# Kernel tuning notes

Hardware: AMD Instinct MI355X
Metric: run time of the kernel (lower is better)

## Reference

```python
import jax, jax.numpy as jnp
import numpy as np

B, N, F_IN, T = 4, 512, 64, 16
K, F_CHEB, F_TIME, TS = 3, 64, 64, 1
E = 16384
LN_EPS = 1e-5


def setup_inputs() -> dict:
    key = jax.random.key(0)
    ks = jax.random.split(key, 18)
    s = 0.05
    X = jax.random.normal(ks[0], (B, N, F_IN, T), jnp.float32)
    # edges with guaranteed no self-loops (so remove_self_loops is a no-op)
    src = jax.random.randint(ks[1], (E,), 0, N, jnp.int32)
    off = jax.random.randint(ks[2], (E,), 1, N, jnp.int32)
    dst = (src + off) % N
    edge_index = jnp.stack([src, dst])
    return {
        'X': X,
        'edge_index': edge_index,
        'U1': jax.random.uniform(ks[3], (N,)) * s,
        'U2': jax.random.normal(ks[4], (F_IN, N)) * s,
        'U3': jax.random.uniform(ks[5], (F_IN,)) * s,
        'be': jax.random.normal(ks[6], (1, T, T)) * s,
        'Ve': jax.random.normal(ks[7], (T, T)) * s,
        'Ws1': jax.random.uniform(ks[8], (T,)) * s,
        'Ws2': jax.random.normal(ks[9], (F_IN, T)) * s,
        'Ws3': jax.random.uniform(ks[10], (F_IN,)) * s,
        'bs': jax.random.normal(ks[11], (1, N, N)) * s,
        'Vs': jax.random.normal(ks[12], (N, N)) * s,
        'W_cheb': jax.random.normal(ks[13], (K, F_IN, F_CHEB)) * s,
        'b_cheb': jax.random.uniform(ks[14], (F_CHEB,)) * s,
        'Wt': jax.random.normal(ks[15], (F_TIME, F_CHEB, 1, 3)) * s,
        'bt': jnp.zeros((F_TIME,), jnp.float32),
        'Wr': jax.random.normal(ks[16], (F_TIME, F_IN, 1, 1)) * s,
        'br': jnp.zeros((F_TIME,), jnp.float32),
        'gamma': jnp.ones((F_TIME,), jnp.float32),
        'beta': jnp.zeros((F_TIME,), jnp.float32),
    }


def _forward(edge_index, X, U1, U2, U3, be, Ve, Ws1, Ws2, Ws3, bs, Vs,
             W_cheb, b_cheb, Wt, bt, Wr, br, gamma, beta):
    Bn, Nn, Fn, Tn = X.shape
    # ---- temporal attention: (B,T,T)
    lhs_t = jnp.einsum('bnft,n->btf', X, U1) @ U2            # (B,T,N)
    rhs_t = jnp.einsum('f,bnft->bnt', U3, X)                 # (B,N,T)
    Et = jnp.matmul(Ve, jax.nn.sigmoid(jnp.matmul(lhs_t, rhs_t) + be))
    Et = jax.nn.softmax(Et, axis=1)
    # temporally re-weighted signal
    Xt = jnp.matmul(X.reshape(Bn, Nn * Fn, Tn), Et).reshape(Bn, Nn, Fn, Tn)
    # ---- spatial attention: (B,N,N)
    lhs_s = jnp.einsum('bnft,t->bnf', Xt, Ws1) @ Ws2         # (B,N,T)
    rhs_s = jnp.einsum('f,bnft->btn', Ws3, Xt)               # (B,T,N)
    S = jnp.matmul(Vs, jax.nn.sigmoid(jnp.matmul(lhs_s, rhs_s) + bs))
    S = jax.nn.softmax(S, axis=1)                            # (B,N,N)
    # ---- scaled sym-normalized Laplacian; lambda_max=2 so 2/lambda_max = 1.
    # edges: -D^-1/2 A D^-1/2 (E), +I self loops (N), then add_self_loops(-1) (N)
    row, col = edge_index[0], edge_index[1]
    ew = jnp.ones(row.shape, X.dtype)
    deg = jnp.zeros((Nn,), X.dtype).at[row].add(ew)
    dis = jnp.where(deg > 0, 1.0 / jnp.sqrt(jnp.maximum(deg, 1.0)), 0.0)  # deg is integral so max() only guards deg==0
    wn = -dis[row] * dis[col]
    loops = jnp.arange(Nn)
    rows = jnp.concatenate([row, loops, loops])
    cols = jnp.concatenate([col, loops, loops])
    norm = jnp.concatenate([wn, jnp.ones((Nn,), X.dtype), -jnp.ones((Nn,), X.dtype)])
    att_norm = norm[None, :] * S[:, rows, cols]              # (B,Etot)

    def prop(h, w):
        # propagate over transposed edges: gather at col, scatter-add at row
        # h: (B,T,N,F); w broadcastable to (B,1,Etot)
        msg = w[..., None] * h[:, :, cols, :]
        return jnp.zeros_like(h).at[:, :, rows, :].add(msg)

    xt = X.transpose(0, 3, 1, 2)                             # (B,T,N,F): ChebConv applied per timestep
    Tx0 = jnp.diagonal(S, axis1=1, axis2=2)[:, None, :, None] * xt  # diag(S) @ x
    out = jnp.einsum('btnf,fg->btng', Tx0, W_cheb[0])
    if W_cheb.shape[0] > 1:
        Tx1 = prop(Tx0, att_norm[:, None, :])
        out = out + jnp.einsum('btnf,fg->btng', Tx1, W_cheb[1])
    for k in range(2, W_cheb.shape[0]):
        Tx2 = 2.0 * prop(Tx1, norm[None, None, :]) - Tx0
        out = out + jnp.einsum('btnf,fg->btng', Tx2, W_cheb[k])
        Tx0, Tx1 = Tx1, Tx2
    X_hat = jax.nn.relu(out + b_cheb)                        # (B,T,N,Fc)
    # ---- time conv (1x3, stride (1,TS)) on (B,Fc,N,T) + residual 1x1 conv
    conv_t = jax.lax.conv_general_dilated(
        X_hat.transpose(0, 3, 2, 1), Wt, (1, TS), ((0, 0), (1, 1)),
        dimension_numbers=('NCHW', 'OIHW', 'NCHW')) + bt[None, :, None, None]
    conv_r = jax.lax.conv_general_dilated(
        X.transpose(0, 2, 1, 3), Wr, (1, TS), ((0, 0), (0, 0)),
        dimension_numbers=('NCHW', 'OIHW', 'NCHW')) + br[None, :, None, None]
    Z = jax.nn.relu(conv_r + conv_t).transpose(0, 3, 2, 1)   # (B,T,N,Ft)
    mu = jnp.mean(Z, -1, keepdims=True)
    var = jnp.var(Z, -1, keepdims=True)
    Z = (Z - mu) / jnp.sqrt(var + LN_EPS) * gamma + beta     # LayerNorm over Ft
    return Z.transpose(0, 2, 3, 1)                           # (B,N,Ft,T)


def reference(X, edge_index, U1, U2, U3, be, Ve, Ws1, Ws2, Ws3, bs, Vs,
              W_cheb, b_cheb, Wt, bt, Wr, br, gamma, beta):
    return _forward(edge_index, X, U1, U2, U3, be, Ve, Ws1, Ws2, Ws3, bs, Vs,
                    W_cheb, b_cheb, Wt, bt, Wr, br, gamma, beta)
```

## Files before the change

### kernel.cpp

```cpp
#include <hip/hip_runtime.h>
#include <math.h>

#define NB 4
#define NV 512
#define NF 64
#define NT 16
#define NE 16384

#define TX1_OFF    2097152u
#define TX2_OFF    4194304u
#define XHAT_OFF   6291456u
#define ST_OFF     TX1_OFF
#define SIGT_OFF   TX2_OFF
#define BST_OFF    8388608u
#define ET_OFF     8650752u
#define PART_OFF   8651776u
#define RHST_OFF   8684544u
#define LHSS_OFF   8717312u
#define RHSSN_OFF  8750080u
#define DIAGS_OFF  8782848u
#define WSATT_OFF  8784896u
#define CSRW_OFF   8850432u
#define WTT_OFF    8866816u
#define WRT_OFF    8879104u
#define DIS_OFF    8883200u
#define RHS3_OFF   8883712u
#define EW1_OFF    8916480u
#define FEND       8916544u

__global__ void k_hist(const int* __restrict__ row, int* __restrict__ counts) {
    __shared__ int h[512];
    int c = blockIdx.x, i = threadIdx.x;
    h[i] = 0; h[i + 256] = 0;
    __syncthreads();
    atomicAdd(&h[row[c * 256 + i]], 1);
    __syncthreads();
    counts[c * 512 + i] = h[i];
    counts[c * 512 + i + 256] = h[i + 256];
}

__global__ void k_scan2(int* __restrict__ counts, float* __restrict__ dis,
                        int* __restrict__ row_start) {
    __shared__ int sc[512];
    int r = threadIdx.x;
    int sum = 0;
    for (int c = 0; c < 64; ++c) {
        int v = counts[c * 512 + r];
        counts[c * 512 + r] = sum;
        sum += v;
    }
    dis[r] = sum > 0 ? 1.0f / sqrtf((float)sum) : 0.0f;
    sc[r] = sum;
    __syncthreads();
    for (int off = 1; off < 512; off <<= 1) {
        int v = sc[r];
        int add = (r >= off) ? sc[r - off] : 0;
        __syncthreads();
        sc[r] = v + add;
        __syncthreads();
    }
    int incl = sc[r];
    row_start[r] = incl - sum;
    if (r == 511) row_start[512] = incl;
}

__global__ void k_fill2(const int* __restrict__ ei, const int* __restrict__ counts,
                        const int* __restrict__ row_start, const float* __restrict__ dis,
                        int* __restrict__ csr_col, int* __restrict__ csr_row,
                        float* __restrict__ csr_w) {
    __shared__ int rowL[256];
    int c = blockIdx.x, i = threadIdx.x;
    int e = c * 256 + i;
    int r = ei[e];
    int col = ei[NE + e];
    rowL[i] = r;
    __syncthreads();
    int rank = 0;
    for (int j = 0; j < 256; ++j)
        if (j < i && rowL[j] == r) rank++;
    int pos = row_start[r] + counts[c * 512 + r] + rank;
    csr_col[pos] = col;
    csr_row[pos] = r;
    csr_w[pos] = -dis[r] * dis[col];
}

__global__ void k_wtrans(const float* __restrict__ Wt, const float* __restrict__ Wr,
                         const float* __restrict__ bs,
                         float* __restrict__ WtT, float* __restrict__ WrT,
                         float* __restrict__ bsT) {
    __shared__ float tile[64][65];
    int bid = blockIdx.x;
    if (bid < 64) {
        int r0 = (bid >> 3) * 64, c0 = (bid & 7) * 64;
        int c = threadIdx.x & 63, rq = threadIdx.x >> 6;
        for (int k = 0; k < 16; ++k) {
            int r = rq * 16 + k;
            tile[r][c] = bs[(r0 + r) * 512 + c0 + c];
        }
        __syncthreads();
        int r2 = threadIdx.x & 63;
        for (int k = 0; k < 16; ++k) {
            int c2 = rq * 16 + k;
            bsT[(size_t)(c0 + c2) * 512 + r0 + r2] = tile[r2][c2];
        }
    } else {
        int idx = (bid - 64) * 256 + threadIdx.x;
        if (idx < 12288) {
            int o = idx & 63, gd = idx >> 6;
            int g = gd / 3, dt = gd - g * 3;
            WtT[idx] = Wt[(o * 64 + g) * 3 + dt];
        } else if (idx < 16384) {
            int i2 = idx - 12288;
            int o = i2 & 63, f = i2 >> 6;
            WrT[i2] = Wr[o * 64 + f];
        }
    }
}

__global__ void k_xin(const float* __restrict__ X, const float* __restrict__ U1,
                      const float* __restrict__ U3, const float* __restrict__ Ws3,
                      float* __restrict__ part, float* __restrict__ rhs,
                      float* __restrict__ rhs3) {
    int bid = blockIdx.x;
    int tid = threadIdx.x;
    if (bid < 32) {
        int b = bid >> 3, g = bid & 7;
        float acc[4] = {0.f, 0.f, 0.f, 0.f};
        const float* Xb = X + (size_t)b * NV * 1024;
        int n0 = g * 64;
        for (int nn = 0; nn < 64; ++nn) {
            int n = n0 + nn;
            float u = U1[n];
            const float* xp = Xb + (size_t)n * 1024;
#pragma unroll
            for (int k = 0; k < 4; ++k) acc[k] += xp[tid + 256 * k] * u;
        }
#pragma unroll
        for (int k = 0; k < 4; ++k) part[(size_t)(b * 8 + g) * 1024 + tid + 256 * k] = acc[k];
    } else {
        int gid = (bid - 32) * 256 + tid;
        int t = gid & 15;
        const float* xp = X + ((size_t)(gid >> 4)) * 1024 + t;
        float a = 0.f, a3 = 0.f;
#pragma unroll
        for (int f = 0; f < 64; ++f) {
            float v = xp[f * 16];
            a += U3[f] * v;
            a3 += Ws3[f] * v;
        }
        rhs[gid] = a;
        rhs3[gid] = a3;
    }
}

__global__ void k_temporal(const float* __restrict__ part, const float* __restrict__ rhs_g,
                           const float* __restrict__ U2, const float* __restrict__ be,
                           const float* __restrict__ Ve, const float* __restrict__ Ws1,
                           float* __restrict__ Et, float* __restrict__ ew1) {
    __shared__ float lhs1[1024];
    __shared__ float rhsL[8192];
    __shared__ float M[1024];
    __shared__ float Esig[256];
    __shared__ float Et0[256];
    __shared__ float red[32];
    __shared__ float EtL[256];
    int b = blockIdx.x, tid = threadIdx.x;
#pragma unroll
    for (int k = 0; k < 4; ++k) {
        int idx = tid + 256 * k;
        float s = 0.f;
        for (int g = 0; g < 8; ++g) s += part[(size_t)(b * 8 + g) * 1024 + idx];
        lhs1[idx] = s;
    }
    for (int k = 0; k < 32; ++k) rhsL[tid + 256 * k] = rhs_g[(size_t)b * 8192 + tid + 256 * k];
    __syncthreads();
    {
        float acc[4] = {0.f, 0.f, 0.f, 0.f};
        int fA[4], tA[4];
#pragma unroll
        for (int k = 0; k < 4; ++k) { int idx = tid + 256 * k; fA[k] = idx >> 4; tA[k] = idx & 15; }
        for (int n = 0; n < 512; ++n) {
#pragma unroll
            for (int k = 0; k < 4; ++k) acc[k] += U2[fA[k] * 512 + n] * rhsL[n * 16 + tA[k]];
        }
#pragma unroll
        for (int k = 0; k < 4; ++k) M[tid + 256 * k] = acc[k];
    }
    __syncthreads();
    {
        int t1 = tid >> 4, t2 = tid & 15;
        float s = 0.f;
        for (int f = 0; f < 64; ++f) s += lhs1[f * 16 + t1] * M[f * 16 + t2];
        s += be[t1 * 16 + t2];
        Esig[tid] = 1.f / (1.f + expf(-s));
    }
    __syncthreads();
    {
        int t1 = tid >> 4, t2 = tid & 15;
        float s = 0.f;
        for (int k = 0; k < 16; ++k) s += Ve[t1 * 16 + k] * Esig[k * 16 + t2];
        Et0[tid] = s;
    }
    __syncthreads();
    if (tid < 16) {
        float m = -1e30f;
        for (int k = 0; k < 16; ++k) m = fmaxf(m, Et0[k * 16 + tid]);
        float s = 0.f;
        for (int k = 0; k < 16; ++k) s += expf(Et0[k * 16 + tid] - m);
        red[tid] = m; red[16 + tid] = 1.f / s;
    }
    __syncthreads();
    {
        int t2 = tid & 15;
        float etv = expf(Et0[tid] - red[t2]) * red[16 + t2];
        Et[b * 256 + tid] = etv;
        EtL[tid] = etv;
    }
    __syncthreads();
    if (tid < 16) {
        float s = 0.f;
        for (int t = 0; t < 16; ++t) s += EtL[tid * 16 + t] * Ws1[t];
        ew1[b * 16 + tid] = s;
    }
}

__global__ __launch_bounds__(256) void k_spat2(const float* __restrict__ X,
                                               const float* __restrict__ ew1,
                                               const float* __restrict__ rhs3,
                                               const float* __restrict__ Et,
                                               const float* __restrict__ Ws2,
                                               float* __restrict__ lhs_s,
                                               float* __restrict__ rhs_sn) {
    int wv = threadIdx.x >> 6, lane = threadIdx.x & 63;
    int bn = blockIdx.x * 4 + wv;
    int b = bn >> 9;
    const float4* xp = (const float4*)(X + (size_t)bn * 1024 + lane * 16);
    float4 x0 = xp[0], x1 = xp[1], x2 = xp[2], x3 = xp[3];
    const float* e1 = ew1 + b * 16;
    float l1 = x0.x * e1[0] + x0.y * e1[1] + x0.z * e1[2] + x0.w * e1[3]
             + x1.x * e1[4] + x1.y * e1[5] + x1.z * e1[6] + x1.w * e1[7]
             + x2.x * e1[8] + x2.y * e1[9] + x2.z * e1[10] + x2.w * e1[11]
             + x3.x * e1[12] + x3.y * e1[13] + x3.z * e1[14] + x3.w * e1[15];
    const float4* wp = (const float4*)(Ws2 + lane * 16);
    float4 w0 = wp[0], w1 = wp[1], w2 = wp[2], w3 = wp[3];
    float p[16] = {l1 * w0.x, l1 * w0.y, l1 * w0.z, l1 * w0.w,
                   l1 * w1.x, l1 * w1.y, l1 * w1.z, l1 * w1.w,
                   l1 * w2.x, l1 * w2.y, l1 * w2.z, l1 * w2.w,
                   l1 * w3.x, l1 * w3.y, l1 * w3.z, l1 * w3.w};
#pragma unroll
    for (int off = 32; off; off >>= 1) {
#pragma unroll
        for (int k = 0; k < 16; ++k) p[k] += __shfl_xor(p[k], off);
    }
    if (lane == 0) {
        float4* lp = (float4*)(lhs_s + (size_t)bn * 16);
        lp[0] = make_float4(p[0], p[1], p[2], p[3]);
        lp[1] = make_float4(p[4], p[5], p[6], p[7]);
        lp[2] = make_float4(p[8], p[9], p[10], p[11]);
        lp[3] = make_float4(p[12], p[13], p[14], p[15]);
    }
    if (lane < 16) {
        const float* r3 = rhs3 + (size_t)bn * 16;
        const float* Eb = Et + b * 256;
        float s = 0.f;
#pragma unroll
        for (int tp = 0; tp < 16; ++tp) s += r3[tp] * Eb[tp * 16 + lane];
        rhs_sn[(size_t)bn * 16 + lane] = s;
    }
}

__global__ void k_sigT(const float* __restrict__ lhs_s, const float* __restrict__ rhs_sn,
                       const float* __restrict__ bsT, float* __restrict__ sigT) {
    int gid = blockIdx.x * 256 + threadIdx.x;
    int k = gid & 511, j = (gid >> 9) & 511, b = gid >> 18;
    const float4* lp = (const float4*)(lhs_s + (size_t)(b * 512 + k) * 16);
    const float4* rp = (const float4*)(rhs_sn + (size_t)(b * 512 + j) * 16);
    float s = 0.f;
#pragma unroll
    for (int q = 0; q < 4; ++q) {
        float4 a = lp[q], c = rp[q];
        s += a.x * c.x + a.y * c.y + a.z * c.z + a.w * c.w;
    }
    s += bsT[(size_t)j * 512 + k];
    sigT[gid] = 1.f / (1.f + expf(-s));
}

__global__ __launch_bounds__(256) void k_gemm_s(const float* __restrict__ sigT,
                                                const float* __restrict__ Vs,
                                                float* __restrict__ S0T) {
    __shared__ float As[32 * 68];
    __shared__ float Bs[32 * 68];
    int bI = blockIdx.x, bJ = blockIdx.y, b = blockIdx.z;
    int tid = threadIdx.x, tx = tid & 15, ty = tid >> 4;
    float acc[4][4] = {};
    const float* Ab = sigT + ((size_t)b * 512 + bJ * 64) * 512;
    const float* Bb = Vs + (size_t)bI * 64 * 512;
    for (int k0 = 0; k0 < 512; k0 += 32) {
#pragma unroll
        for (int p = 0; p < 2; ++p) {
            int idx = tid + 256 * p;
            int row = idx >> 3, kk = (idx & 7) * 4;
            float4 a = *(const float4*)(Ab + (size_t)row * 512 + k0 + kk);
            As[(kk + 0) * 68 + row] = a.x; As[(kk + 1) * 68 + row] = a.y;
            As[(kk + 2) * 68 + row] = a.z; As[(kk + 3) * 68 + row] = a.w;
            float4 v = *(const float4*)(Bb + (size_t)row * 512 + k0 + kk);
            Bs[(kk + 0) * 68 + row] = v.x; Bs[(kk + 1) * 68 + row] = v.y;
            Bs[(kk + 2) * 68 + row] = v.z; Bs[(kk + 3) * 68 + row] = v.w;
        }
        __syncthreads();
#pragma unroll
        for (int kk = 0; kk < 32; ++kk) {
            float4 a = *(const float4*)(As + kk * 68 + ty * 4);
            float4 bv = *(const float4*)(Bs + kk * 68 + tx * 4);
            acc[0][0] += a.x * bv.x; acc[0][1] += a.x * bv.y; acc[0][2] += a.x * bv.z; acc[0][3] += a.x * bv.w;
            acc[1][0] += a.y * bv.x; acc[1][1] += a.y * bv.y; acc[1][2] += a.y * bv.z; acc[1][3] += a.y * bv.w;
            acc[2][0] += a.z * bv.x; acc[2][1] += a.z * bv.y; acc[2][2] += a.z * bv.z; acc[2][3] += a.z * bv.w;
            acc[3][0] += a.w * bv.x; acc[3][1] += a.w * bv.y; acc[3][2] += a.w * bv.z; acc[3][3] += a.w * bv.w;
        }
        __syncthreads();
    }
    float* Cb = S0T + ((size_t)b * 512 + bJ * 64) * 512 + bI * 64;
#pragma unroll
    for (int y = 0; y < 4; ++y) {
        int j = ty * 4 + y;
        *(float4*)(Cb + (size_t)j * 512 + tx * 4) =
            make_float4(acc[y][0], acc[y][1], acc[y][2], acc[y][3]);
    }
}

__global__ void k_softmax_s(float* __restrict__ ST, float* __restrict__ diagS) {
    __shared__ float red[4];
    int bj = blockIdx.x;
    int b = bj >> 9, j = bj & 511;
    float* row = ST + (size_t)bj * 512;
    int tid = threadIdx.x;
    float v0 = row[tid], v1 = row[tid + 256];
    float m = fmaxf(v0, v1);
    for (int off = 32; off; off >>= 1) m = fmaxf(m, __shfl_xor(m, off));
    if ((tid & 63) == 0) red[tid >> 6] = m;
    __syncthreads();
    m = fmaxf(fmaxf(red[0], red[1]), fmaxf(red[2], red[3]));
    __syncthreads();
    float e0 = expf(v0 - m), e1 = expf(v1 - m);
    float s = e0 + e1;
    for (int off = 32; off; off >>= 1) s += __shfl_xor(s, off);
    if ((tid & 63) == 0) red[tid >> 6] = s;
    __syncthreads();
    s = red[0] + red[1] + red[2] + red[3];
    float inv = 1.f / s;
    float r0 = e0 * inv, r1 = e1 * inv;
    row[tid] = r0;
    row[tid + 256] = r1;
    if (j < 256) { if (tid == j) diagS[b * 512 + j] = r0; }
    else { if (tid == j - 256) diagS[b * 512 + j] = r1; }
}

__global__ void k_wS(const int* __restrict__ csr_col, const int* __restrict__ csr_row,
                     const float* __restrict__ csr_w, const float* __restrict__ ST,
                     const float* __restrict__ diagS, float* __restrict__ wS) {
    int gid = blockIdx.x * 256 + threadIdx.x;
    int pos = gid & (NE - 1), b = gid >> 14;
    int c = csr_col[pos], r = csr_row[pos];
    wS[gid] = csr_w[pos] * ST[((size_t)(b * 512 + c)) * 512 + r] * diagS[b * 512 + c];
}

__global__ __launch_bounds__(256) void k_prop1(const float* __restrict__ X,
                                               const float* __restrict__ wS,
                                               const int* __restrict__ csr_col,
                                               const int* __restrict__ row_start,
                                               float* __restrict__ Tx1) {
    int logical = ((blockIdx.x & 7) << 8) + (blockIdx.x >> 3);
    int b = logical >> 9, tile = (logical >> 7) & 3, rq = logical & 127;
    int w = threadIdx.x >> 6, lane = threadIdx.x & 63;
    int i = rq * 4 + w;
    int s = row_start[i], e2 = row_start[i + 1];
    const float* Xb = X + (size_t)b * 512 * 1024 + tile * 256 + lane * 4;
    const float* wb = wS + (size_t)b * NE;
    float4 acc = make_float4(0.f, 0.f, 0.f, 0.f);
    for (int p = s; p < e2; ++p) {
        int col = csr_col[p];
        float wv = wb[p];
        float4 v = *(const float4*)(Xb + (size_t)col * 1024);
        acc.x += wv * v.x; acc.y += wv * v.y; acc.z += wv * v.z; acc.w += wv * v.w;
    }
    *(float4*)(Tx1 + ((size_t)(b * 512 + i)) * 1024 + tile * 256 + lane * 4) = acc;
}

__global__ __launch_bounds__(256) void k_prop2(const float* __restrict__ Tx1,
                                               const float* __restrict__ X,
                                               const float* __restrict__ diagS,
                                               const float* __restrict__ csr_w,
                                               const int* __restrict__ csr_col,
                                               const int* __restrict__ row_start,
                                               float* __restrict__ Tx2) {
    int logical = ((blockIdx.x & 7) << 8) + (blockIdx.x >> 3);
    int b = logical >> 9, tile = (logical >> 7) & 3, rq = logical & 127;
    int w = threadIdx.x >> 6, lane = threadIdx.x & 63;
    int i = rq * 4 + w;
    int s = row_start[i], e2 = row_start[i + 1];
    const float* T1b = Tx1 + (size_t)b * 512 * 1024 + tile * 256 + lane * 4;
    float4 acc = make_float4(0.f, 0.f, 0.f, 0.f);
    for (int p = s; p < e2; ++p) {
        int col = csr_col[p];
        float wv = csr_w[p];
        float4 v = *(const float4*)(T1b + (size_t)col * 1024);
        acc.x += wv * v.x; acc.y += wv * v.y; acc.z += wv * v.z; acc.w += wv * v.w;
    }
    float ds = diagS[b * 512 + i];
    size_t off = ((size_t)(b * 512 + i)) * 1024 + tile * 256 + lane * 4;
    float4 x0 = *(const float4*)(X + off);
    float4 o;
    o.x = 2.f * acc.x - ds * x0.x;
    o.y = 2.f * acc.y - ds * x0.y;
    o.z = 2.f * acc.z - ds * x0.z;
    o.w = 2.f * acc.w - ds * x0.w;
    *(float4*)(Tx2 + off) = o;
}

__global__ __launch_bounds__(256) void k_cheb(const float* __restrict__ X,
                                              const float* __restrict__ Tx1,
                                              const float* __restrict__ Tx2,
                                              const float* __restrict__ diagS,
                                              const float* __restrict__ Wc,
                                              const float* __restrict__ bc,
                                              float* __restrict__ Xh) {
    __shared__ float t0s[4][1024], t1s[4][1024], t2s[4][1024];
    int bn0 = blockIdx.x * 4;
    int tid = threadIdx.x;
    int r = tid >> 6, l = tid & 63;
    int bn = bn0 + r;
    float ds = diagS[bn];
    const float4* xp = (const float4*)(X + (size_t)bn * 1024);
    const float4* p1 = (const float4*)(Tx1 + (size_t)bn * 1024);
    const float4* p2 = (const float4*)(Tx2 + (size_t)bn * 1024);
#pragma unroll
    for (int k = 0; k < 4; ++k) {
        float4 v = xp[k * 64 + l];
        v.x *= ds; v.y *= ds; v.z *= ds; v.w *= ds;
        ((float4*)t0s[r])[k * 64 + l] = v;
        ((float4*)t1s[r])[k * 64 + l] = p1[k * 64 + l];
        ((float4*)t2s[r])[k * 64 + l] = p2[k * 64 + l];
    }
    __syncthreads();
    int g4 = (l & 15) * 4, t4 = (l >> 4) * 4;
    float4 bv = *(const float4*)(bc + g4);
    float4 acc0 = make_float4(bv.x, bv.x, bv.x, bv.x);
    float4 acc1 = make_float4(bv.y, bv.y, bv.y, bv.y);
    float4 acc2 = make_float4(bv.z, bv.z, bv.z, bv.z);
    float4 acc3 = make_float4(bv.w, bv.w, bv.w, bv.w);
    const float* t0r = t0s[r];
    const float* t1r = t1s[r];
    const float* t2r = t2s[r];
    for (int f = 0; f < 64; ++f) {
        float4 a0 = *(const float4*)(t0r + f * 16 + t4);
        float4 a1 = *(const float4*)(t1r + f * 16 + t4);
        float4 a2 = *(const float4*)(t2r + f * 16 + t4);
        float4 w0 = *(const float4*)(Wc + f * 64 + g4);
        float4 w1 = *(const float4*)(Wc + 4096 + f * 64 + g4);
        float4 w2 = *(const float4*)(Wc + 8192 + f * 64 + g4);
        acc0.x += w0.x * a0.x + w1.x * a1.x + w2.x * a2.x;
        acc0.y += w0.x * a0.y + w1.x * a1.y + w2.x * a2.y;
        acc0.z += w0.x * a0.z + w1.x * a1.z + w2.x * a2.z;
        acc0.w += w0.x * a0.w + w1.x * a1.w + w2.x * a2.w;
        acc1.x += w0.y * a0.x + w1.y * a1.x + w2.y * a2.x;
        acc1.y += w0.y * a0.y + w1.y * a1.y + w2.y * a2.y;
        acc1.z += w0.y * a0.z + w1.y * a1.z + w2.y * a2.z;
        acc1.w += w0.y * a0.w + w1.y * a1.w + w2.y * a2.w;
        acc2.x += w0.z * a0.x + w1.z * a1.x + w2.z * a2.x;
        acc2.y += w0.z * a0.y + w1.z * a1.y + w2.z * a2.y;
        acc2.z += w0.z * a0.z + w1.z * a1.z + w2.z * a2.z;
        acc2.w += w0.z * a0.w + w1.z * a1.w + w2.z * a2.w;
        acc3.x += w0.w * a0.x + w1.w * a1.x + w2.w * a2.x;
        acc3.y += w0.w * a0.y + w1.w * a1.y + w2.w * a2.y;
        acc3.z += w0.w * a0.z + w1.w * a1.z + w2.w * a2.z;
        acc3.w += w0.w * a0.w + w1.w * a1.w + w2.w * a2.w;
    }
    float* op = Xh + (size_t)bn * 1024;
    float4 o0, o1, o2, o3;
    o0.x = fmaxf(acc0.x, 0.f); o0.y = fmaxf(acc0.y, 0.f); o0.z = fmaxf(acc0.z, 0.f); o0.w = fmaxf(acc0.w, 0.f);
    o1.x = fmaxf(acc1.x, 0.f); o1.y = fmaxf(acc1.y, 0.f); o1.z = fmaxf(acc1.z, 0.f); o1.w = fmaxf(acc1.w, 0.f);
    o2.x = fmaxf(acc2.x, 0.f); o2.y = fmaxf(acc2.y, 0.f); o2.z = fmaxf(acc2.z, 0.f); o2.w = fmaxf(acc2.w, 0.f);
    o3.x = fmaxf(acc3.x, 0.f); o3.y = fmaxf(acc3.y, 0.f); o3.z = fmaxf(acc3.z, 0.f); o3.w = fmaxf(acc3.w, 0.f);
    *(float4*)(op + (g4 + 0) * 16 + t4) = o0;
    *(float4*)(op + (g4 + 1) * 16 + t4) = o1;
    *(float4*)(op + (g4 + 2) * 16 + t4) = o2;
    *(float4*)(op + (g4 + 3) * 16 + t4) = o3;
}

__global__ __launch_bounds__(256) void k_out(const float* __restrict__ X,
                                             const float* __restrict__ Xh,
                                             const float* __restrict__ WtT,
                                             const float* __restrict__ WrT,
                                             const float* __restrict__ bt,
                                             const float* __restrict__ br,
                                             const float* __restrict__ gamma,
                                             const float* __restrict__ beta,
                                             float* __restrict__ out) {
    __shared__ float xh[64 * 20];
    __shared__ float xl[64 * 16];
    __shared__ float red[4160];
    int bn = blockIdx.x;
    int tid = threadIdx.x;
    int o = tid & 63, q = tid >> 6;
    {
        int g = tid & 63, s4 = tid >> 6;
        int slot = (s4 == 0) ? 0 : 16 + s4;
        xh[g * 20 + slot] = 0.f;
    }
    {
        float4 v = ((const float4*)(Xh + (size_t)bn * 1024))[tid];
        int g = tid >> 2, t0 = (tid & 3) * 4;
        xh[g * 20 + t0 + 1] = v.x;
        xh[g * 20 + t0 + 2] = v.y;
        xh[g * 20 + t0 + 3] = v.z;
        xh[g * 20 + t0 + 4] = v.w;
        float4 u = ((const float4*)(X + (size_t)bn * 1024))[tid];
        *(float4*)(xl + tid * 4) = u;
    }
    __syncthreads();
    float acc[16];
#pragma unroll
    for (int k = 0; k < 16; ++k) acc[k] = 0.f;
    for (int gi = 0; gi < 16; ++gi) {
        int g = q * 16 + gi;
        const float4* xp = (const float4*)(xh + g * 20);
        float4 xa = xp[0], xb = xp[1], xc = xp[2], xd = xp[3], xe = xp[4];
        float xs[20] = {xa.x, xa.y, xa.z, xa.w, xb.x, xb.y, xb.z, xb.w,
                        xc.x, xc.y, xc.z, xc.w, xd.x, xd.y, xd.z, xd.w,
                        xe.x, xe.y, xe.z, xe.w};
        float w0 = WtT[(g * 3 + 0) * 64 + o];
        float w1 = WtT[(g * 3 + 1) * 64 + o];
        float w2 = WtT[(g * 3 + 2) * 64 + o];
#pragma unroll
        for (int tt = 0; tt < 16; ++tt)
            acc[tt] += xs[tt] * w0 + xs[tt + 1] * w1 + xs[tt + 2] * w2;
    }
    for (int fi = 0; fi < 16; ++fi) {
        int f = q * 16 + fi;
        const float4* xp = (const float4*)(xl + f * 16);
        float4 xa = xp[0], xb = xp[1], xc = xp[2], xd = xp[3];
        float xs[16] = {xa.x, xa.y, xa.z, xa.w, xb.x, xb.y, xb.z, xb.w,
                        xc.x, xc.y, xc.z, xc.w, xd.x, xd.y, xd.z, xd.w};
        float w = WrT[f * 64 + o];
#pragma unroll
        for (int tt = 0; tt < 16; ++tt) acc[tt] += xs[tt] * w;
    }
#pragma unroll
    for (int tt = 0; tt < 16; ++tt) red[q * 1024 + tt * 64 + o] = acc[tt];
    __syncthreads();
    float bsum = bt[o] + br[o];
    float go = gamma[o], bo = beta[o];
    float zv4[4];
#pragma unroll
    for (int tt = 0; tt < 4; ++tt) {
        int t = q * 4 + tt;
        float s = bsum;
#pragma unroll
        for (int qq = 0; qq < 4; ++qq) s += red[qq * 1024 + t * 64 + o];
        zv4[tt] = fmaxf(s, 0.f);
    }
    __syncthreads();
#pragma unroll
    for (int tt = 0; tt < 4; ++tt) {
        int t = q * 4 + tt;
        float zv = zv4[tt];
        float s = zv, sq = zv * zv;
        for (int off = 32; off; off >>= 1) {
            s += __shfl_xor(s, off);
            sq += __shfl_xor(sq, off);
        }
        float mu = s * (1.f / 64.f);
        float var = sq * (1.f / 64.f) - mu * mu;
        red[t * 65 + o] = (zv - mu) * rsqrtf(var + 1e-5f) * go + bo;
    }
    __syncthreads();
#pragma unroll
    for (int k = 0; k < 4; ++k) {
        int i = tid + 256 * k;
        out[(size_t)bn * 1024 + i] = red[(i & 15) * 65 + (i >> 4)];
    }
}

extern "C" void kernel_launch(void* const* d_in, const int* in_sizes, int n_in,
                              void* d_out, int out_size, void* d_ws, size_t ws_size,
                              hipStream_t stream) {
    const float* X     = (const float*)d_in[0];
    const int*   ei    = (const int*)d_in[1];
    const float* U1    = (const float*)d_in[2];
    const float* U2    = (const float*)d_in[3];
    const float* U3    = (const float*)d_in[4];
    const float* be    = (const float*)d_in[5];
    const float* Ve    = (const float*)d_in[6];
    const float* Ws1   = (const float*)d_in[7];
    const float* Ws2   = (const float*)d_in[8];
    const float* Ws3   = (const float*)d_in[9];
    const float* bs    = (const float*)d_in[10];
    const float* Vs    = (const float*)d_in[11];
    const float* Wc    = (const float*)d_in[12];
    const float* bc    = (const float*)d_in[13];
    const float* Wt    = (const float*)d_in[14];
    const float* bt    = (const float*)d_in[15];
    const float* Wr    = (const float*)d_in[16];
    const float* br    = (const float*)d_in[17];
    const float* gamma = (const float*)d_in[18];
    const float* beta  = (const float*)d_in[19];

    float* ws = (float*)d_ws;
    float* Tx1    = ws + TX1_OFF;
    float* Tx2    = ws + TX2_OFF;
    float* Xh     = ws + XHAT_OFF;
    float* ST     = ws + ST_OFF;
    float* sigT   = ws + SIGT_OFF;
    float* bsT    = ws + BST_OFF;
    float* Et     = ws + ET_OFF;
    float* part   = ws + PART_OFF;
    float* rhs_t  = ws + RHST_OFF;
    float* lhs_s  = ws + LHSS_OFF;
    float* rhs_sn = ws + RHSSN_OFF;
    float* diagS  = ws + DIAGS_OFF;
    float* wS     = ws + WSATT_OFF;
    float* csr_w  = ws + CSRW_OFF;
    float* WtT    = ws + WTT_OFF;
    float* WrT    = ws + WRT_OFF;
    float* dis    = ws + DIS_OFF;
    float* rhs3   = ws + RHS3_OFF;
    float* ew1    = ws + EW1_OFF;

    int* ib        = (int*)(ws + FEND);
    int* row_start = ib;
    int* csr_col   = ib + 516;
    int* csr_row   = csr_col + NE;
    int* counts    = csr_row + NE;

    k_hist<<<64, 256, 0, stream>>>(ei, counts);
    k_scan2<<<1, 512, 0, stream>>>(counts, dis, row_start);
    k_fill2<<<64, 256, 0, stream>>>(ei, counts, row_start, dis, csr_col, csr_row, csr_w);

    k_wtrans<<<128, 256, 0, stream>>>(Wt, Wr, bs, WtT, WrT, bsT);

    k_xin<<<160, 256, 0, stream>>>(X, U1, U3, Ws3, part, rhs_t, rhs3);
    k_temporal<<<4, 256, 0, stream>>>(part, rhs_t, U2, be, Ve, Ws1, Et, ew1);

    k_spat2<<<512, 256, 0, stream>>>(X, ew1, rhs3, Et, Ws2, lhs_s, rhs_sn);
    k_sigT<<<4096, 256, 0, stream>>>(lhs_s, rhs_sn, bsT, sigT);
    k_gemm_s<<<dim3(8, 8, 4), 256, 0, stream>>>(sigT, Vs, ST);
    k_softmax_s<<<2048, 256, 0, stream>>>(ST, diagS);
    k_wS<<<256, 256, 0, stream>>>(csr_col, csr_row, csr_w, ST, diagS, wS);

    k_prop1<<<2048, 256, 0, stream>>>(X, wS, csr_col, row_start, Tx1);
    k_prop2<<<2048, 256, 0, stream>>>(Tx1, X, diagS, csr_w, csr_col, row_start, Tx2);
    k_cheb<<<512, 256, 0, stream>>>(X, Tx1, Tx2, diagS, Wc, bc, Xh);

    k_out<<<2048, 256, 0, stream>>>(X, Xh, WtT, WrT, bt, br, gamma, beta, (float*)d_out);
}
```

Baseline: 181.2 us.

## Fuse prop2, Chebyshev combine and output conv into one tail kernel; merge prep kernels

```diff
diff --git a/kernel.cpp b/kernel.cpp
--- a/kernel.cpp
+++ b/kernel.cpp
@@ -9,7 +9,6 @@
 
 #define TX1_OFF    2097152u
 #define TX2_OFF    4194304u
-#define XHAT_OFF   6291456u
 #define ST_OFF     TX1_OFF
 #define SIGT_OFF   TX2_OFF
 #define BST_OFF    8388608u
@@ -28,15 +27,82 @@
 #define EW1_OFF    8916480u
 #define FEND       8916544u
 
-__global__ void k_hist(const int* __restrict__ row, int* __restrict__ counts) {
+__global__ void k_prep(const int* __restrict__ ei, int* __restrict__ counts,
+                       const float* __restrict__ Wt, const float* __restrict__ Wr,
+                       const float* __restrict__ bs,
+                       float* __restrict__ WtT, float* __restrict__ WrT,
+                       float* __restrict__ bsT,
+                       const float* __restrict__ X, const float* __restrict__ U1,
+                       const float* __restrict__ U3, const float* __restrict__ Ws3,
+                       float* __restrict__ part, float* __restrict__ rhs,
+                       float* __restrict__ rhs3) {
     __shared__ int h[512];
-    int c = blockIdx.x, i = threadIdx.x;
-    h[i] = 0; h[i + 256] = 0;
-    __syncthreads();
-    atomicAdd(&h[row[c * 256 + i]], 1);
-    __syncthreads();
-    counts[c * 512 + i] = h[i];
-    counts[c * 512 + i + 256] = h[i + 256];
+    __shared__ float tile[64][65];
+    int bid = blockIdx.x, tid = threadIdx.x;
+    if (bid < 64) {
+        int c = bid;
+        h[tid] = 0; h[tid + 256] = 0;
+        __syncthreads();
+        atomicAdd(&h[ei[c * 256 + tid]], 1);
+        __syncthreads();
+        counts[c * 512 + tid] = h[tid];
+        counts[c * 512 + tid + 256] = h[tid + 256];
+    } else if (bid < 128) {
+        int tb = bid - 64;
+        int r0 = (tb >> 3) * 64, c0 = (tb & 7) * 64;
+        int c = tid & 63, rq = tid >> 6;
+        for (int k = 0; k < 16; ++k) {
+            int r = rq * 16 + k;
+            tile[r][c] = bs[(r0 + r) * 512 + c0 + c];
+        }
+        __syncthreads();
+        int r2 = tid & 63;
+        for (int k = 0; k < 16; ++k) {
+            int c2 = rq * 16 + k;
+            bsT[(size_t)(c0 + c2) * 512 + r0 + r2] = tile[r2][c2];
+        }
+    } else if (bid < 192) {
+        int idx = (bid - 128) * 256 + tid;
+        if (idx < 12288) {
+            int o = idx & 63, gd = idx >> 6;
+            int g = gd / 3, dt = gd - g * 3;
+            WtT[idx] = Wt[(o * 64 + g) * 3 + dt];
+        } else {
+            int i2 = idx - 12288;
+            int o = i2 & 63, f = i2 >> 6;
+            WrT[i2] = Wr[o * 64 + f];
+        }
+    } else {
+        int sub = bid - 192;
+        if (sub < 32) {
+            int b = sub >> 3, g = sub & 7;
+            float acc[4] = {0.f, 0.f, 0.f, 0.f};
+            const float* Xb = X + (size_t)b * NV * 1024;
+            int n0 = g * 64;
+            for (int nn = 0; nn < 64; ++nn) {
+                int n = n0 + nn;
+                float u = U1[n];
+                const float* xp = Xb + (size_t)n * 1024;
+#pragma unroll
+                for (int k = 0; k < 4; ++k) acc[k] += xp[tid + 256 * k] * u;
+            }
+#pragma unroll
+            for (int k = 0; k < 4; ++k) part[(size_t)(b * 8 + g) * 1024 + tid + 256 * k] = acc[k];
+        } else {
+            int gid = (sub - 32) * 256 + tid;
+            int t = gid & 15;
+            const float* xp = X + ((size_t)(gid >> 4)) * 1024 + t;
+            float a = 0.f, a3 = 0.f;
+#pragma unroll
+            for (int f = 0; f < 64; ++f) {
+                float v = xp[f * 16];
+                a += U3[f] * v;
+                a3 += Ws3[f] * v;
+            }
+            rhs[gid] = a;
+            rhs3[gid] = a3;
+        }
+    }
 }
 
 __global__ void k_scan2(int* __restrict__ counts, float* __restrict__ dis,
@@ -82,75 +148,6 @@
     csr_col[pos] = col;
     csr_row[pos] = r;
     csr_w[pos] = -dis[r] * dis[col];
-}
-
-__global__ void k_wtrans(const float* __restrict__ Wt, const float* __restrict__ Wr,
-                         const float* __restrict__ bs,
-                         float* __restrict__ WtT, float* __restrict__ WrT,
-                         float* __restrict__ bsT) {
-    __shared__ float tile[64][65];
-    int bid = blockIdx.x;
-    if (bid < 64) {
-        int r0 = (bid >> 3) * 64, c0 = (bid & 7) * 64;
-        int c = threadIdx.x & 63, rq = threadIdx.x >> 6;
-        for (int k = 0; k < 16; ++k) {
-            int r = rq * 16 + k;
-            tile[r][c] = bs[(r0 + r) * 512 + c0 + c];
-        }
-        __syncthreads();
-        int r2 = threadIdx.x & 63;
-        for (int k = 0; k < 16; ++k) {
-            int c2 = rq * 16 + k;
-            bsT[(size_t)(c0 + c2) * 512 + r0 + r2] = tile[r2][c2];
-        }
-    } else {
-        int idx = (bid - 64) * 256 + threadIdx.x;
-        if (idx < 12288) {
-            int o = idx & 63, gd = idx >> 6;
-            int g = gd / 3, dt = gd - g * 3;
-            WtT[idx] = Wt[(o * 64 + g) * 3 + dt];
-        } else if (idx < 16384) {
-            int i2 = idx - 12288;
-            int o = i2 & 63, f = i2 >> 6;
-            WrT[i2] = Wr[o * 64 + f];
-        }
-    }
-}
-
-__global__ void k_xin(const float* __restrict__ X, const float* __restrict__ U1,
-                      const float* __restrict__ U3, const float* __restrict__ Ws3,
-                      float* __restrict__ part, float* __restrict__ rhs,
-                      float* __restrict__ rhs3) {
-    int bid = blockIdx.x;
-    int tid = threadIdx.x;
-    if (bid < 32) {
-        int b = bid >> 3, g = bid & 7;
-        float acc[4] = {0.f, 0.f, 0.f, 0.f};
-        const float* Xb = X + (size_t)b * NV * 1024;
-        int n0 = g * 64;
-        for (int nn = 0; nn < 64; ++nn) {
-            int n = n0 + nn;
-            float u = U1[n];
-            const float* xp = Xb + (size_t)n * 1024;
-#pragma unroll
-            for (int k = 0; k < 4; ++k) acc[k] += xp[tid + 256 * k] * u;
-        }
-#pragma unroll
-        for (int k = 0; k < 4; ++k) part[(size_t)(b * 8 + g) * 1024 + tid + 256 * k] = acc[k];
-    } else {
-        int gid = (bid - 32) * 256 + tid;
-        int t = gid & 15;
-        const float* xp = X + ((size_t)(gid >> 4)) * 1024 + t;
-        float a = 0.f, a3 = 0.f;
-#pragma unroll
-        for (int f = 0; f < 64; ++f) {
-            float v = xp[f * 16];
-            a += U3[f] * v;
-            a3 += Ws3[f] * v;
-        }
-        rhs[gid] = a;
-        rhs3[gid] = a3;
-    }
 }
 
 __global__ void k_temporal(const float* __restrict__ part, const float* __restrict__ rhs_g,
@@ -386,19 +383,31 @@
     *(float4*)(Tx1 + ((size_t)(b * 512 + i)) * 1024 + tile * 256 + lane * 4) = acc;
 }
 
-__global__ __launch_bounds__(256) void k_prop2(const float* __restrict__ Tx1,
-                                               const float* __restrict__ X,
-                                               const float* __restrict__ diagS,
-                                               const float* __restrict__ csr_w,
-                                               const int* __restrict__ csr_col,
-                                               const int* __restrict__ row_start,
-                                               float* __restrict__ Tx2) {
-    int logical = ((blockIdx.x & 7) << 8) + (blockIdx.x >> 3);
-    int b = logical >> 9, tile = (logical >> 7) & 3, rq = logical & 127;
-    int w = threadIdx.x >> 6, lane = threadIdx.x & 63;
-    int i = rq * 4 + w;
+__global__ __launch_bounds__(256) void k_tail(const float* __restrict__ X,
+                                              const float* __restrict__ Tx1,
+                                              const float* __restrict__ diagS,
+                                              const float* __restrict__ csr_w,
+                                              const int* __restrict__ csr_col,
+                                              const int* __restrict__ row_start,
+                                              const float* __restrict__ Wc,
+                                              const float* __restrict__ bc,
+                                              const float* __restrict__ WtT,
+                                              const float* __restrict__ WrT,
+                                              const float* __restrict__ bt,
+                                              const float* __restrict__ br,
+                                              const float* __restrict__ gamma,
+                                              const float* __restrict__ beta,
+                                              float* __restrict__ out) {
+    __shared__ float t0s[1024], t1s[1024], t2s[1024], xl[1024];
+    __shared__ float xh[1280];
+    __shared__ float red[4160];
+    int blk = ((blockIdx.x & 7) << 8) + (blockIdx.x >> 3);
+    int b = blk >> 9, i = blk & 511;
+    int tid = threadIdx.x;
+#pragma unroll
+    for (int k = 0; k < 5; ++k) xh[tid + 256 * k] = 0.f;
     int s = row_start[i], e2 = row_start[i + 1];
-    const float* T1b = Tx1 + (size_t)b * 512 * 1024 + tile * 256 + lane * 4;
+    const float* T1b = Tx1 + (size_t)b * 512 * 1024 + tid * 4;
     float4 acc = make_float4(0.f, 0.f, 0.f, 0.f);
     for (int p = s; p < e2; ++p) {
         int col = csr_col[p];
@@ -406,121 +415,47 @@
         float4 v = *(const float4*)(T1b + (size_t)col * 1024);
         acc.x += wv * v.x; acc.y += wv * v.y; acc.z += wv * v.z; acc.w += wv * v.w;
     }
-    float ds = diagS[b * 512 + i];
-    size_t off = ((size_t)(b * 512 + i)) * 1024 + tile * 256 + lane * 4;
-    float4 x0 = *(const float4*)(X + off);
-    float4 o;
-    o.x = 2.f * acc.x - ds * x0.x;
-    o.y = 2.f * acc.y - ds * x0.y;
-    o.z = 2.f * acc.z - ds * x0.z;
-    o.w = 2.f * acc.w - ds * x0.w;
-    *(float4*)(Tx2 + off) = o;
-}
-
-__global__ __launch_bounds__(256) void k_cheb(const float* __restrict__ X,
-                                              const float* __restrict__ Tx1,
-                                              const float* __restrict__ Tx2,
-                                              const float* __restrict__ diagS,
-                                              const float* __restrict__ Wc,
-                                              const float* __restrict__ bc,
-                                              float* __restrict__ Xh) {
-    __shared__ float t0s[4][1024], t1s[4][1024], t2s[4][1024];
-    int bn0 = blockIdx.x * 4;
-    int tid = threadIdx.x;
-    int r = tid >> 6, l = tid & 63;
-    int bn = bn0 + r;
-    float ds = diagS[bn];
-    const float4* xp = (const float4*)(X + (size_t)bn * 1024);
-    const float4* p1 = (const float4*)(Tx1 + (size_t)bn * 1024);
-    const float4* p2 = (const float4*)(Tx2 + (size_t)bn * 1024);
-#pragma unroll
-    for (int k = 0; k < 4; ++k) {
-        float4 v = xp[k * 64 + l];
-        v.x *= ds; v.y *= ds; v.z *= ds; v.w *= ds;
-        ((float4*)t0s[r])[k * 64 + l] = v;
-        ((float4*)t1s[r])[k * 64 + l] = p1[k * 64 + l];
-        ((float4*)t2s[r])[k * 64 + l] = p2[k * 64 + l];
-    }
-    __syncthreads();
-    int g4 = (l & 15) * 4, t4 = (l >> 4) * 4;
-    float4 bv = *(const float4*)(bc + g4);
-    float4 acc0 = make_float4(bv.x, bv.x, bv.x, bv.x);
-    float4 acc1 = make_float4(bv.y, bv.y, bv.y, bv.y);
-    float4 acc2 = make_float4(bv.z, bv.z, bv.z, bv.z);
-    float4 acc3 = make_float4(bv.w, bv.w, bv.w, bv.w);
-    const float* t0r = t0s[r];
-    const float* t1r = t1s[r];
-    const float* t2r = t2s[r];
-    for (int f = 0; f < 64; ++f) {
-        float4 a0 = *(const float4*)(t0r + f * 16 + t4);
-        float4 a1 = *(const float4*)(t1r + f * 16 + t4);
-        float4 a2 = *(const float4*)(t2r + f * 16 + t4);
-        float4 w0 = *(const float4*)(Wc + f * 64 + g4);
-        float4 w1 = *(const float4*)(Wc + 4096 + f * 64 + g4);
-        float4 w2 = *(const float4*)(Wc + 8192 + f * 64 + g4);
-        acc0.x += w0.x * a0.x + w1.x * a1.x + w2.x * a2.x;
-        acc0.y += w0.x * a0.y + w1.x * a1.y + w2.x * a2.y;
-        acc0.z += w0.x * a0.z + w1.x * a1.z + w2.x * a2.z;
-        acc0.w += w0.x * a0.w + w1.x * a1.w + w2.x * a2.w;
-        acc1.x += w0.y * a0.x + w1.y * a1.x + w2.y * a2.x;
-        acc1.y += w0.y * a0.y + w1.y * a1.y + w2.y * a2.y;
-        acc1.z += w0.y * a0.z + w1.y * a1.z + w2.y * a2.z;
-        acc1.w += w0.y * a0.w + w1.y * a1.w + w2.y * a2.w;
-        acc2.x += w0.z * a0.x + w1.z * a1.x + w2.z * a2.x;
-        acc2.y += w0.z * a0.y + w1.z * a1.y + w2.z * a2.y;
-        acc2.z += w0.z * a0.z + w1.z * a1.z + w2.z * a2.z;
-        acc2.w += w0.z * a0.w + w1.z * a1.w + w2.z * a2.w;
-        acc3.x += w0.w * a0.x + w1.w * a1.x + w2.w * a2.x;
-        acc3.y += w0.w * a0.y + w1.w * a1.y + w2.w * a2.y;
-        acc3.z += w0.w * a0.z + w1.w * a1.z + w2.w * a2.z;
-        acc3.w += w0.w * a0.w + w1.w * a1.w + w2.w * a2.w;
-    }
-    float* op = Xh + (size_t)bn * 1024;
-    float4 o0, o1, o2, o3;
-    o0.x = fmaxf(acc0.x, 0.f); o0.y = fmaxf(acc0.y, 0.f); o0.z = fmaxf(acc0.z, 0.f); o0.w = fmaxf(acc0.w, 0.f);
-    o1.x = fmaxf(acc1.x, 0.f); o1.y = fmaxf(acc1.y, 0.f); o1.z = fmaxf(acc1.z, 0.f); o1.w = fmaxf(acc1.w, 0.f);
-    o2.x = fmaxf(acc2.x, 0.f); o2.y = fmaxf(acc2.y, 0.f); o2.z = fmaxf(acc2.z, 0.f); o2.w = fmaxf(acc2.w, 0.f);
-    o3.x = fmaxf(acc3.x, 0.f); o3.y = fmaxf(acc3.y, 0.f); o3.z = fmaxf(acc3.z, 0.f); o3.w = fmaxf(acc3.w, 0.f);
-    *(float4*)(op + (g4 + 0) * 16 + t4) = o0;
-    *(float4*)(op + (g4 + 1) * 16 + t4) = o1;
-    *(float4*)(op + (g4 + 2) * 16 + t4) = o2;
-    *(float4*)(op + (g4 + 3) * 16 + t4) = o3;
-}
-
-__global__ __launch_bounds__(256) void k_out(const float* __restrict__ X,
-                                             const float* __restrict__ Xh,
-                                             const float* __restrict__ WtT,
-                                             const float* __restrict__ WrT,
-                                             const float* __restrict__ bt,
-                                             const float* __restrict__ br,
-                                             const float* __restrict__ gamma,
-                                             const float* __restrict__ beta,
-                                             float* __restrict__ out) {
-    __shared__ float xh[64 * 20];
-    __shared__ float xl[64 * 16];
-    __shared__ float red[4160];
-    int bn = blockIdx.x;
-    int tid = threadIdx.x;
+    float ds = diagS[blk];
+    size_t roff = (size_t)blk * 1024 + tid * 4;
+    float4 x0 = *(const float4*)(X + roff);
+    float4 t1v = *(const float4*)(Tx1 + roff);
+    float4 t2v, t0v;
+    t2v.x = 2.f * acc.x - ds * x0.x;
+    t2v.y = 2.f * acc.y - ds * x0.y;
+    t2v.z = 2.f * acc.z - ds * x0.z;
+    t2v.w = 2.f * acc.w - ds * x0.w;
+    t0v.x = ds * x0.x; t0v.y = ds * x0.y; t0v.z = ds * x0.z; t0v.w = ds * x0.w;
+    *(float4*)(xl  + tid * 4) = x0;
+    *(float4*)(t0s + tid * 4) = t0v;
+    *(float4*)(t1s + tid * 4) = t1v;
+    *(float4*)(t2s + tid * 4) = t2v;
+    __syncthreads();
+    {
+        int g4 = (tid & 15) * 4, t = tid >> 4;
+        float4 bv = *(const float4*)(bc + g4);
+        float4 accg = bv;
+        for (int f = 0; f < 64; ++f) {
+            float a0 = t0s[f * 16 + t];
+            float a1 = t1s[f * 16 + t];
+            float a2 = t2s[f * 16 + t];
+            float4 w0 = *(const float4*)(Wc + f * 64 + g4);
+            float4 w1 = *(const float4*)(Wc + 4096 + f * 64 + g4);
+            float4 w2 = *(const float4*)(Wc + 8192 + f * 64 + g4);
+            accg.x += w0.x * a0 + w1.x * a1 + w2.x * a2;
+            accg.y += w0.y * a0 + w1.y * a1 + w2.y * a2;
+            accg.z += w0.z * a0 + w1.z * a1 + w2.z * a2;
+            accg.w += w0.w * a0 + w1.w * a1 + w2.w * a2;
+        }
+        xh[(g4 + 0) * 20 + t + 1] = fmaxf(accg.x, 0.f);
+        xh[(g4 + 1) * 20 + t + 1] = fmaxf(accg.y, 0.f);
+        xh[(g4 + 2) * 20 + t + 1] = fmaxf(accg.z, 0.f);
+        xh[(g4 + 3) * 20 + t + 1] = fmaxf(accg.w, 0.f);
+    }
+    __syncthreads();
     int o = tid & 63, q = tid >> 6;
-    {
-        int g = tid & 63, s4 = tid >> 6;
-        int slot = (s4 == 0) ? 0 : 16 + s4;
-        xh[g * 20 + slot] = 0.f;
-    }
-    {
-        float4 v = ((const float4*)(Xh + (size_t)bn * 1024))[tid];
-        int g = tid >> 2, t0 = (tid & 3) * 4;
-        xh[g * 20 + t0 + 1] = v.x;
-        xh[g * 20 + t0 + 2] = v.y;
-        xh[g * 20 + t0 + 3] = v.z;
-        xh[g * 20 + t0 + 4] = v.w;
-        float4 u = ((const float4*)(X + (size_t)bn * 1024))[tid];
-        *(float4*)(xl + tid * 4) = u;
-    }
-    __syncthreads();
-    float acc[16];
-#pragma unroll
-    for (int k = 0; k < 16; ++k) acc[k] = 0.f;
+    float accv[16];
+#pragma unroll
+    for (int k = 0; k < 16; ++k) accv[k] = 0.f;
     for (int gi = 0; gi < 16; ++gi) {
         int g = q * 16 + gi;
         const float4* xp = (const float4*)(xh + g * 20);
@@ -533,7 +468,7 @@
         float w2 = WtT[(g * 3 + 2) * 64 + o];
 #pragma unroll
         for (int tt = 0; tt < 16; ++tt)
-            acc[tt] += xs[tt] * w0 + xs[tt + 1] * w1 + xs[tt + 2] * w2;
+            accv[tt] += xs[tt] * w0 + xs[tt + 1] * w1 + xs[tt + 2] * w2;
     }
     for (int fi = 0; fi < 16; ++fi) {
         int f = q * 16 + fi;
@@ -543,10 +478,10 @@
                         xc.x, xc.y, xc.z, xc.w, xd.x, xd.y, xd.z, xd.w};
         float w = WrT[f * 64 + o];
 #pragma unroll
-        for (int tt = 0; tt < 16; ++tt) acc[tt] += xs[tt] * w;
-    }
-#pragma unroll
-    for (int tt = 0; tt < 16; ++tt) red[q * 1024 + tt * 64 + o] = acc[tt];
+        for (int tt = 0; tt < 16; ++tt) accv[tt] += xs[tt] * w;
+    }
+#pragma unroll
+    for (int tt = 0; tt < 16; ++tt) red[q * 1024 + tt * 64 + o] = accv[tt];
     __syncthreads();
     float bsum = bt[o] + br[o];
     float go = gamma[o], bo = beta[o];
@@ -554,30 +489,30 @@
 #pragma unroll
     for (int tt = 0; tt < 4; ++tt) {
         int t = q * 4 + tt;
-        float s = bsum;
-#pragma unroll
-        for (int qq = 0; qq < 4; ++qq) s += red[qq * 1024 + t * 64 + o];
-        zv4[tt] = fmaxf(s, 0.f);
+        float sv = bsum;
+#pragma unroll
+        for (int qq = 0; qq < 4; ++qq) sv += red[qq * 1024 + t * 64 + o];
+        zv4[tt] = fmaxf(sv, 0.f);
     }
     __syncthreads();
 #pragma unroll
     for (int tt = 0; tt < 4; ++tt) {
         int t = q * 4 + tt;
         float zv = zv4[tt];
-        float s = zv, sq = zv * zv;
+        float sv = zv, sq = zv * zv;
         for (int off = 32; off; off >>= 1) {
-            s += __shfl_xor(s, off);
+            sv += __shfl_xor(sv, off);
             sq += __shfl_xor(sq, off);
         }
-        float mu = s * (1.f / 64.f);
+        float mu = sv * (1.f / 64.f);
         float var = sq * (1.f / 64.f) - mu * mu;
         red[t * 65 + o] = (zv - mu) * rsqrtf(var + 1e-5f) * go + bo;
     }
     __syncthreads();
 #pragma unroll
     for (int k = 0; k < 4; ++k) {
-        int i = tid + 256 * k;
-        out[(size_t)bn * 1024 + i] = red[(i & 15) * 65 + (i >> 4)];
+        int idx = tid + 256 * k;
+        out[(size_t)blk * 1024 + idx] = red[(idx & 15) * 65 + (idx >> 4)];
     }
 }
 
@@ -607,8 +542,6 @@
 
     float* ws = (float*)d_ws;
     float* Tx1    = ws + TX1_OFF;
-    float* Tx2    = ws + TX2_OFF;
-    float* Xh     = ws + XHAT_OFF;
     float* ST     = ws + ST_OFF;
     float* sigT   = ws + SIGT_OFF;
     float* bsT    = ws + BST_OFF;
@@ -632,13 +565,11 @@
     int* csr_row   = csr_col + NE;
     int* counts    = csr_row + NE;
 
-    k_hist<<<64, 256, 0, stream>>>(ei, counts);
+    k_prep<<<352, 256, 0, stream>>>(ei, counts, Wt, Wr, bs, WtT, WrT, bsT,
+                                    X, U1, U3, Ws3, part, rhs_t, rhs3);
     k_scan2<<<1, 512, 0, stream>>>(counts, dis, row_start);
     k_fill2<<<64, 256, 0, stream>>>(ei, counts, row_start, dis, csr_col, csr_row, csr_w);
 
-    k_wtrans<<<128, 256, 0, stream>>>(Wt, Wr, bs, WtT, WrT, bsT);
-
-    k_xin<<<160, 256, 0, stream>>>(X, U1, U3, Ws3, part, rhs_t, rhs3);
     k_temporal<<<4, 256, 0, stream>>>(part, rhs_t, U2, be, Ve, Ws1, Et, ew1);
 
     k_spat2<<<512, 256, 0, stream>>>(X, ew1, rhs3, Et, Ws2, lhs_s, rhs_sn);
@@ -648,8 +579,7 @@
     k_wS<<<256, 256, 0, stream>>>(csr_col, csr_row, csr_w, ST, diagS, wS);
 
     k_prop1<<<2048, 256, 0, stream>>>(X, wS, csr_col, row_start, Tx1);
-    k_prop2<<<2048, 256, 0, stream>>>(Tx1, X, diagS, csr_w, csr_col, row_start, Tx2);
-    k_cheb<<<512, 256, 0, stream>>>(X, Tx1, Tx2, diagS, Wc, bc, Xh);
-
-    k_out<<<2048, 256, 0, stream>>>(X, Xh, WtT, WrT, bt, br, gamma, beta, (float*)d_out);
-}
+    k_tail<<<2048, 256, 0, stream>>>(X, Tx1, diagS, csr_w, csr_col, row_start,
+                                     Wc, bc, WtT, WrT, bt, br, gamma, beta,
+                                     (float*)d_out);
+}
```

New measurement: 180.6 us. About the same (-0.3%).
